# Optimization experiments

Measured on AMD Instinct MI355X. Metric: run time of the kernel, lower is better.

The kernel has to match this reference:

```python
import jax, jax.numpy as jnp
import numpy as np

N_NODES = 50000
N_EDGES = 800000
IN_FEATS = 128
OUT_CLASSES = 128


def _glorot(key, shape):
    fan_in, fan_out = shape[1], shape[0]
    limit = float(np.sqrt(6.0 / (fan_in + fan_out)))
    return jax.random.uniform(key, shape, jnp.float32, -limit, limit)


def setup_inputs() -> dict:
    key = jax.random.key(0)
    ks = jax.random.split(key, 11)
    x = jax.random.normal(ks[0], (N_NODES, IN_FEATS), jnp.float32)
    edge_index = jax.random.randint(ks[1], (2, N_EDGES), 0, N_NODES, jnp.int64)
    h = OUT_CLASSES // 2
    # PyG SAGEConv: lin_l applied to aggregated neighbors (has bias), lin_r to root (no bias)
    return {
        "x": x,
        "edge_index": edge_index,
        "W_l1": _glorot(ks[2], (OUT_CLASSES, IN_FEATS)),
        "b1": jnp.zeros((OUT_CLASSES,), jnp.float32),
        "W_r1": _glorot(ks[3], (OUT_CLASSES, IN_FEATS)),
        "W_l2": _glorot(ks[4], (h, OUT_CLASSES)),
        "b2": jnp.zeros((h,), jnp.float32),
        "W_r2": _glorot(ks[5], (h, OUT_CLASSES)),
        "W_l3": _glorot(ks[6], (OUT_CLASSES, h)),
        "b3": jnp.zeros((OUT_CLASSES,), jnp.float32),
        "W_r3": _glorot(ks[7], (OUT_CLASSES, h)),
    }


def _sage_conv(x, src, dst, W_l, b, W_r):
    # gather source-node features, mean-aggregate at destinations
    msgs = x[src]                                               # [E, d]
    agg = jax.ops.segment_sum(msgs, dst, num_segments=N_NODES)  # [N, d]
    cnt = jax.ops.segment_sum(jnp.ones((src.shape[0], 1), x.dtype), dst,
                              num_segments=N_NODES)             # [N, 1]
    mean = agg / jnp.maximum(cnt, 1.0)
    return mean @ W_l.T + b + x @ W_r.T


def reference(x, edge_index, W_l1, b1, W_r1, W_l2, b2, W_r2, W_l3, b3, W_r3):
    src, dst = edge_index[0], edge_index[1]
    h = _sage_conv(x, src, dst, W_l1, b1, W_r1)
    h = _sage_conv(h, src, dst, W_l2, b2, W_r2)
    h = _sage_conv(h, src, dst, W_l3, b3, W_r3)
    return h
```

## Files before the change

kernel.cpp:

```cpp
#include <hip/hip_runtime.h>

#define N_NODES 50000
#define N_EDGES 800000
#define BUCKETS 196
#define ECHUNK 4096
#define EBLKS 196
#define BCAP 5120

typedef __attribute__((ext_vector_type(8))) _Float16 half8;
typedef __attribute__((ext_vector_type(4))) _Float16 half4;
typedef __attribute__((ext_vector_type(4))) float f32x4;

template <int E> struct hvec;
template <> struct hvec<8> { typedef half8 t; };
template <> struct hvec<4> { typedef half4 t; };


template <int L, int E, int DEPTH>
__device__ __forceinline__ void gather_sum(const _Float16* __restrict__ feat,
                                           const unsigned short* __restrict__ csr,
                                           int start, int d, int lane,
                                           float* acc) {
  using V = typename hvec<E>::t;
  const V* ip = (const V*)feat;
  if (d <= 0) return;
  int nb = (d + DEPTH - 1) / DEPTH;
  int sc[DEPTH];
#pragma unroll
  for (int j = 0; j < DEPTH; ++j) sc[j] = csr[start + (j < d ? j : d - 1)];
  V vlast;
  for (int b = 0; b < nb; ++b) {
    V v[DEPTH];
#pragma unroll
    for (int j = 0; j < DEPTH; ++j) v[j] = ip[(size_t)sc[j] * L + lane];
    int e2 = (b + 1) * DEPTH;
    if (e2 < d) {
#pragma unroll
      for (int j = 0; j < DEPTH; ++j) {
        int idx = e2 + j;
        sc[j] = csr[start + (idx < d ? idx : d - 1)];
      }
    }
#pragma unroll
    for (int j = 0; j < DEPTH; ++j)
#pragma unroll
      for (int q = 0; q < E; ++q) acc[q] += (float)v[j][q];
    vlast = v[DEPTH - 1];
  }
  int rem = d - (nb - 1) * DEPTH;
  if (rem < DEPTH) {
    float corr = (float)(DEPTH - rem);
#pragma unroll
    for (int q = 0; q < E; ++q) acc[q] -= corr * (float)vlast[q];
  }
}


__global__ __launch_bounds__(256) void prep_k(
    const int* __restrict__ src, const int* __restrict__ dst,
    int* __restrict__ gcur, unsigned* __restrict__ binned,
    const float* __restrict__ x, _Float16* __restrict__ xh,
    const float* __restrict__ Wl1, const float* __restrict__ Wr1,
    const float* __restrict__ Wl2, const float* __restrict__ Wr2,
    const float* __restrict__ Wl3, const float* __restrict__ Wr3,
    _Float16* ph_l1, _Float16* pl_l1, _Float16* ph_r1, _Float16* pl_r1,
    _Float16* ph_c2, _Float16* pl_c2, _Float16* ph_l3, _Float16* pl_l3,
    _Float16* ph_r3, _Float16* pl_r3) {
  int blk = blockIdx.x;
  int t = threadIdx.x;
  if (blk < EBLKS) {
    __shared__ int h[BUCKETS];
    __shared__ int base[BUCKETS];
    for (int i = t; i < BUCKETS; i += 256) h[i] = 0;
    __syncthreads();
    int e0 = blk * ECHUNK;
    int eend = e0 + ECHUNK < N_EDGES ? e0 + ECHUNK : N_EDGES;
    for (int e = e0 + t; e < eend; e += 256) atomicAdd(&h[dst[e] >> 8], 1);
    __syncthreads();
    for (int i = t; i < BUCKETS; i += 256) {
      if (h[i]) base[i] = atomicAdd(&gcur[i], h[i]);
      h[i] = 0;
    }
    __syncthreads();
    for (int e = e0 + t; e < eend; e += 256) {
      int d = dst[e];
      int b = d >> 8;
      int r = atomicAdd(&h[b], 1);
      binned[(size_t)b * BCAP + base[b] + r] =
          (unsigned)src[e] | ((unsigned)(d & 255) << 16);
    }
  } else if (blk < EBLKS + 32) {
    int g = (blk - EBLKS) * 256 + t;
    const float *S0, *S1 = nullptr;
    _Float16 *ph, *pl;
    int f, K;
    if (g < 2048)      { f = g;        ph = ph_l1; pl = pl_l1; S0 = Wl1; K = 128; }
    else if (g < 4096) { f = g - 2048; ph = ph_r1; pl = pl_r1; S0 = Wr1; K = 128; }
    else if (g < 6144) { f = g - 4096; ph = ph_c2; pl = pl_c2; S0 = Wl2; S1 = Wr2; K = 128; }
    else if (g < 7168) { f = g - 6144; ph = ph_l3; pl = pl_l3; S0 = Wl3; K = 64; }
    else               { f = g - 7168; ph = ph_r3; pl = pl_r3; S0 = Wr3; K = 64; }
    int kb = f >> 9;
    int rem = f & 511;
    int n = rem >> 2;
    int lq = rem & 3;
    const float* srow =
        (S1 && n >= 64) ? (S1 + (size_t)(n - 64) * K) : (S0 + (size_t)n * K);
    int kbase = kb * 32 + lq * 8;
#pragma unroll
    for (int j = 0; j < 8; ++j) {
      float v = srow[kbase + j];
      _Float16 hi = (_Float16)v;
      ph[f * 8 + j] = hi;
      pl[f * 8 + j] = (_Float16)(v - (float)hi);
    }
  } else {
    int i = (blk - EBLKS - 32) * 256 + t;
    if (i >= N_NODES * 16) return;
    const float4* xp = (const float4*)x;
    float4 a = xp[2 * i];
    float4 b = xp[2 * i + 1];
    half8 hh;
    hh[0] = (_Float16)a.x; hh[1] = (_Float16)a.y; hh[2] = (_Float16)a.z; hh[3] = (_Float16)a.w;
    hh[4] = (_Float16)b.x; hh[5] = (_Float16)b.y; hh[6] = (_Float16)b.z; hh[7] = (_Float16)b.w;
    int node = i >> 4;
    int part = i & 15;
    ((half8*)xh)[(size_t)(part >> 2) * (N_NODES * 4) + (size_t)node * 4 + (part & 3)] = hh;
  }
}

__global__ __launch_bounds__(256) void bucket_fill_k(const unsigned* __restrict__ binned,
                                                     const int* __restrict__ gcnt,
                                                     int* __restrict__ offs,
                                                     int* __restrict__ deg,
                                                     unsigned short* __restrict__ csr) {
  __shared__ int cnt[256];
  __shared__ int loc[256];
  __shared__ int cur[256];
  int b = blockIdx.x;
  int t = threadIdx.x;
  int base = b * BCAP;
  int end = base + gcnt[b];
  cnt[t] = 0;
  __syncthreads();
  for (int e = base + t; e < end; e += 256) atomicAdd(&cnt[(binned[e] >> 16) & 255], 1);
  __syncthreads();
  loc[t] = cnt[t];
  __syncthreads();
  for (int o = 1; o < 256; o <<= 1) {
    int v = (t >= o) ? loc[t - o] : 0;
    __syncthreads();
    loc[t] += v;
    __syncthreads();
  }
  int excl = loc[t] - cnt[t];
  int node = b * 256 + t;
  if (node < N_NODES) {
    offs[node] = base + excl;
    deg[node] = cnt[t];
  }
  cur[t] = excl;
  __syncthreads();
  for (int e = base + t; e < end; e += 256) {
    unsigned r = binned[e];
    int dl = (r >> 16) & 255;
    int p = atomicAdd(&cur[dl], 1);
    csr[base + p] = (unsigned short)(r & 0xFFFF);
  }
}


template <int NSL, bool FUSE, bool OUTSL>
__global__ __launch_bounds__(256, 4) void agg_sliced_k(
    const _Float16* __restrict__ in_sl, _Float16* __restrict__ out,
    const int* __restrict__ offs, const int* __restrict__ deg,
    const unsigned short* __restrict__ csr, const float* __restrict__ bias,
    const _Float16* __restrict__ addend) {
  constexpr int COPIES = 8 / NSL;
  constexpr int F = NSL * 32;
  int g = blockIdx.x & 7;
  int s = g % NSL;
  int chunk = (blockIdx.x >> 3) * COPIES + g / NSL;
  int t = threadIdx.x;
  int node = chunk * 32 + (t >> 3);
  int lane = t & 7;
  if (node >= N_NODES) return;
  const _Float16* base = in_sl + (size_t)s * (N_NODES * 32);
  float acc[4] = {0.f, 0.f, 0.f, 0.f};
  int start = offs[node];
  int d = deg[node];
  gather_sum<8, 4, 16>(base, csr, start, d, lane, acc);
  float inv = d > 0 ? 1.0f / (float)d : 0.0f;
  int feat = s * 32 + lane * 4;
  half4 o;
  if constexpr (FUSE) {
    half4 av = *(const half4*)(addend + (size_t)node * F + feat);
#pragma unroll
    for (int q = 0; q < 4; ++q)
      o[q] = (_Float16)(acc[q] * inv + bias[feat + q] + (float)av[q]);
  } else {
#pragma unroll
    for (int q = 0; q < 4; ++q) o[q] = (_Float16)(acc[q] * inv);
  }
  _Float16* op = OUTSL ? out + (size_t)s * (N_NODES * 32) + (size_t)node * 32 + lane * 4
                       : out + (size_t)node * F + feat;
  *(half4*)op = o;
}


__global__ __launch_bounds__(256, 4) void megagemm_k(
    const _Float16* __restrict__ mh1, const _Float16* __restrict__ xsl,
    const _Float16* __restrict__ Wl1h, const _Float16* __restrict__ Wl1l,
    const _Float16* __restrict__ Wr1h, const _Float16* __restrict__ Wr1l,
    const float* __restrict__ b1,
    const _Float16* __restrict__ Wc2h, const _Float16* __restrict__ Wc2l,
    _Float16* __restrict__ Psl, _Float16* __restrict__ Rh) {
  constexpr int STR = 136;
  __shared__ _Float16 Hsm[16 * STR];
  int t = threadIdx.x;
  int wave = t >> 6;
  int lane = t & 63;
  int l15 = lane & 15;
  int lq = lane >> 4;
  int row0 = blockIdx.x * 16;
  const int woff = (l15 * 4 + lq) * 8;
  int colbase = wave * 32;
  f32x4 acc[2];
  acc[0] = (f32x4){0.f, 0.f, 0.f, 0.f};
  acc[1] = (f32x4){0.f, 0.f, 0.f, 0.f};
  {
    const _Float16* ab = mh1 + (size_t)(row0 + l15) * 128 + lq * 8;
    half8 af[4];
#pragma unroll
    for (int kb = 0; kb < 4; ++kb) af[kb] = *(const half8*)(ab + kb * 32);
#pragma unroll
    for (int kb = 0; kb < 4; ++kb)
#pragma unroll
      for (int ct = 0; ct < 2; ++ct) {
        size_t bi = (size_t)(kb * 128 + colbase + ct * 16) * 32 + woff;
        half8 bh = *(const half8*)(Wl1h + bi);
        half8 bl = *(const half8*)(Wl1l + bi);
        acc[ct] = __builtin_amdgcn_mfma_f32_16x16x32_f16(af[kb], bh, acc[ct], 0, 0, 0);
        acc[ct] = __builtin_amdgcn_mfma_f32_16x16x32_f16(af[kb], bl, acc[ct], 0, 0, 0);
      }
  }
  {
    half8 af[4];
#pragma unroll
    for (int kb = 0; kb < 4; ++kb)
      af[kb] = *(const half8*)(xsl + (size_t)kb * (N_NODES * 32) +
                               (size_t)(row0 + l15) * 32 + lq * 8);
#pragma unroll
    for (int kb = 0; kb < 4; ++kb)
#pragma unroll
      for (int ct = 0; ct < 2; ++ct) {
        size_t bi = (size_t)(kb * 128 + colbase + ct * 16) * 32 + woff;
        half8 bh = *(const half8*)(Wr1h + bi);
        half8 bl = *(const half8*)(Wr1l + bi);
        acc[ct] = __builtin_amdgcn_mfma_f32_16x16x32_f16(af[kb], bh, acc[ct], 0, 0, 0);
        acc[ct] = __builtin_amdgcn_mfma_f32_16x16x32_f16(af[kb], bl, acc[ct], 0, 0, 0);
      }
  }
#pragma unroll
  for (int r = 0; r < 4; ++r) {
    int rl = lq * 4 + r;
#pragma unroll
    for (int ct = 0; ct < 2; ++ct) {
      int col = colbase + ct * 16 + l15;
      Hsm[rl * STR + col] = (_Float16)(acc[ct][r] + b1[col]);
    }
  }
  __syncthreads();
  f32x4 a2[2];
  a2[0] = (f32x4){0.f, 0.f, 0.f, 0.f};
  a2[1] = (f32x4){0.f, 0.f, 0.f, 0.f};
  half8 af[4];
#pragma unroll
  for (int kb = 0; kb < 4; ++kb)
    af[kb] = *(const half8*)&Hsm[l15 * STR + kb * 32 + lq * 8];
#pragma unroll
  for (int kb = 0; kb < 4; ++kb)
#pragma unroll
    for (int ct = 0; ct < 2; ++ct) {
      size_t bi = (size_t)(kb * 128 + colbase + ct * 16) * 32 + woff;
      half8 bh = *(const half8*)(Wc2h + bi);
      half8 bl = *(const half8*)(Wc2l + bi);
      a2[ct] = __builtin_amdgcn_mfma_f32_16x16x32_f16(af[kb], bh, a2[ct], 0, 0, 0);
      a2[ct] = __builtin_amdgcn_mfma_f32_16x16x32_f16(af[kb], bl, a2[ct], 0, 0, 0);
    }
#pragma unroll
  for (int r = 0; r < 4; ++r) {
    int row = row0 + lq * 4 + r;
#pragma unroll
    for (int ct = 0; ct < 2; ++ct) {
      int col = colbase + ct * 16 + l15;
      float v = a2[ct][r];
      if (col < 64)
        Psl[(size_t)(col >> 5) * (N_NODES * 32) + (size_t)row * 32 + (col & 31)] =
            (_Float16)v;
      else
        Rh[(size_t)row * 64 + (col - 64)] = (_Float16)v;
    }
  }
}


__global__ __launch_bounds__(256, 2) void gemm3_k(
    const _Float16* __restrict__ mh3, const _Float16* __restrict__ h2sl,
    const _Float16* __restrict__ Wlh, const _Float16* __restrict__ Wll,
    const _Float16* __restrict__ Wrh, const _Float16* __restrict__ Wrl,
    const float* __restrict__ b3, float* __restrict__ out) {
  int wave = threadIdx.x >> 6;
  int lane = threadIdx.x & 63;
  int l15 = lane & 15;
  int lq = lane >> 4;
  int rowblk = blockIdx.x >> 1;
  int colg = blockIdx.x & 1;
  int rg = rowblk * 4 + wave;
  if (rg >= N_NODES / 16) return;
  int row0 = rg << 4;
  const int woff = (l15 * 4 + lq) * 8;
  f32x4 acc[4];
#pragma unroll
  for (int c = 0; c < 4; ++c) acc[c] = (f32x4){0.f, 0.f, 0.f, 0.f};
  {
    const _Float16* ab = mh3 + (size_t)(row0 + l15) * 64 + lq * 8;
    half8 af[2];
#pragma unroll
    for (int kb = 0; kb < 2; ++kb) af[kb] = *(const half8*)(ab + kb * 32);
#pragma unroll
    for (int kb = 0; kb < 2; ++kb)
#pragma unroll
      for (int ct = 0; ct < 4; ++ct) {
        size_t bi = (size_t)(kb * 128 + colg * 64 + ct * 16) * 32 + woff;
        half8 bh = *(const half8*)(Wlh + bi);
        half8 bl = *(const half8*)(Wll + bi);
        acc[ct] = __builtin_amdgcn_mfma_f32_16x16x32_f16(af[kb], bh, acc[ct], 0, 0, 0);
        acc[ct] = __builtin_amdgcn_mfma_f32_16x16x32_f16(af[kb], bl, acc[ct], 0, 0, 0);
      }
  }
  {
    half8 af[2];
#pragma unroll
    for (int kb = 0; kb < 2; ++kb)
      af[kb] = *(const half8*)(h2sl + (size_t)kb * (N_NODES * 32) +
                               (size_t)(row0 + l15) * 32 + lq * 8);
#pragma unroll
    for (int kb = 0; kb < 2; ++kb)
#pragma unroll
      for (int ct = 0; ct < 4; ++ct) {
        size_t bi = (size_t)(kb * 128 + colg * 64 + ct * 16) * 32 + woff;
        half8 bh = *(const half8*)(Wrh + bi);
        half8 bl = *(const half8*)(Wrl + bi);
        acc[ct] = __builtin_amdgcn_mfma_f32_16x16x32_f16(af[kb], bh, acc[ct], 0, 0, 0);
        acc[ct] = __builtin_amdgcn_mfma_f32_16x16x32_f16(af[kb], bl, acc[ct], 0, 0, 0);
      }
  }
#pragma unroll
  for (int r = 0; r < 4; ++r) {
    int row = row0 + lq * 4 + r;
#pragma unroll
    for (int ct = 0; ct < 4; ++ct) {
      int col = colg * 64 + ct * 16 + l15;
      out[(size_t)row * 128 + col] = acc[ct][r] + b3[col];
    }
  }
}

extern "C" void kernel_launch(void* const* d_in, const int* in_sizes, int n_in,
                              void* d_out, int out_size, void* d_ws, size_t ws_size,
                              hipStream_t stream) {
  const float* x   = (const float*)d_in[0];
  const int* ei    = (const int*)d_in[1];
  const float* Wl1 = (const float*)d_in[2];
  const float* b1  = (const float*)d_in[3];
  const float* Wr1 = (const float*)d_in[4];
  const float* Wl2 = (const float*)d_in[5];
  const float* b2  = (const float*)d_in[6];
  const float* Wr2 = (const float*)d_in[7];
  const float* Wl3 = (const float*)d_in[8];
  const float* b3  = (const float*)d_in[9];
  const float* Wr3 = (const float*)d_in[10];
  float* out = (float*)d_out;

  const int* src = ei;
  const int* dst = ei + N_EDGES;

  char* ws = (char*)d_ws;
  size_t off = 0;
  auto take = [&](size_t bytes) {
    void* p = ws + off;
    off += (bytes + 255) & ~(size_t)255;
    return p;
  };
  int* deg    = (int*)take((size_t)N_NODES * 4);
  int* offs   = (int*)take((size_t)N_NODES * 4);
  int* gcur   = (int*)take((size_t)BUCKETS * 4);
  unsigned* binned = (unsigned*)take((size_t)BUCKETS * BCAP * 4);
  unsigned short* csr = (unsigned short*)take((size_t)BUCKETS * BCAP * 2);
  _Float16* xh   = (_Float16*)take((size_t)N_NODES * 128 * 2);
  _Float16* mh1  = (_Float16*)take((size_t)N_NODES * 128 * 2);
  _Float16* Psl  = (_Float16*)take((size_t)N_NODES * 64 * 2);
  _Float16* Rh   = (_Float16*)take((size_t)N_NODES * 64 * 2);
  _Float16* h2sl = (_Float16*)take((size_t)N_NODES * 64 * 2);
  _Float16* mh3  = (_Float16*)take((size_t)N_NODES * 64 * 2);
  _Float16* ph_l1 = (_Float16*)take(16384 * 2);
  _Float16* pl_l1 = (_Float16*)take(16384 * 2);
  _Float16* ph_r1 = (_Float16*)take(16384 * 2);
  _Float16* pl_r1 = (_Float16*)take(16384 * 2);
  _Float16* ph_c2 = (_Float16*)take(16384 * 2);
  _Float16* pl_c2 = (_Float16*)take(16384 * 2);
  _Float16* ph_l3 = (_Float16*)take(8192 * 2);
  _Float16* pl_l3 = (_Float16*)take(8192 * 2);
  _Float16* ph_r3 = (_Float16*)take(8192 * 2);
  _Float16* pl_r3 = (_Float16*)take(8192 * 2);

  hipMemsetAsync(gcur, 0, (size_t)BUCKETS * 4, stream);

  prep_k<<<EBLKS + 32 + 3125, 256, 0, stream>>>(
      src, dst, gcur, binned, x, xh, Wl1, Wr1, Wl2, Wr2, Wl3, Wr3, ph_l1, pl_l1,
      ph_r1, pl_r1, ph_c2, pl_c2, ph_l3, pl_l3, ph_r3, pl_r3);
  bucket_fill_k<<<BUCKETS, 256, 0, stream>>>(binned, gcur, offs, deg, csr);

  agg_sliced_k<4, false, false><<<8 * 782, 256, 0, stream>>>(
      xh, mh1, offs, deg, csr, nullptr, nullptr);

  megagemm_k<<<3125, 256, 0, stream>>>(mh1, xh, ph_l1, pl_l1, ph_r1, pl_r1, b1,
                                       ph_c2, pl_c2, Psl, Rh);

  agg_sliced_k<2, true, true><<<8 * 391, 256, 0, stream>>>(
      Psl, h2sl, offs, deg, csr, b2, Rh);

  agg_sliced_k<2, false, false><<<8 * 391, 256, 0, stream>>>(
      h2sl, mh3, offs, deg, csr, nullptr, nullptr);

  gemm3_k<<<1564, 256, 0, stream>>>(mh3, h2sl, ph_l3, pl_l3, ph_r3, pl_r3, b3, out);
}
```

Measured before the change: 262.5 us.

## Split fused layer-1/layer-2 GEMM into two kernels via global h1 buffer

Replaces the fused megagemm kernel, which kept the layer-1 output tile in shared memory and fed it straight into the layer-2 projection, with two separate GEMM kernels that pass h1 through a new global fp16 buffer. Each wave now owns a 16-row by 64-column tile with no block-level sync, and launch bounds change to 2 blocks. The intent is likely to drop the __syncthreads and LDS traffic and to rebalance the MFMA work per wave. The cost is an extra kernel launch and a write plus re-read of a 50000x128 fp16 intermediate.

```diff
diff --git a/kernel.cpp b/kernel.cpp
--- a/kernel.cpp
+++ b/kernel.cpp
@@ -207,26 +207,24 @@
 }
 
 
-__global__ __launch_bounds__(256, 4) void megagemm_k(
+__global__ __launch_bounds__(256, 2) void gemm1_k(
     const _Float16* __restrict__ mh1, const _Float16* __restrict__ xsl,
-    const _Float16* __restrict__ Wl1h, const _Float16* __restrict__ Wl1l,
-    const _Float16* __restrict__ Wr1h, const _Float16* __restrict__ Wr1l,
-    const float* __restrict__ b1,
-    const _Float16* __restrict__ Wc2h, const _Float16* __restrict__ Wc2l,
-    _Float16* __restrict__ Psl, _Float16* __restrict__ Rh) {
-  constexpr int STR = 136;
-  __shared__ _Float16 Hsm[16 * STR];
-  int t = threadIdx.x;
-  int wave = t >> 6;
-  int lane = t & 63;
+    const _Float16* __restrict__ Wlh, const _Float16* __restrict__ Wll,
+    const _Float16* __restrict__ Wrh, const _Float16* __restrict__ Wrl,
+    const float* __restrict__ b1, _Float16* __restrict__ h1) {
+  int wave = threadIdx.x >> 6;
+  int lane = threadIdx.x & 63;
   int l15 = lane & 15;
   int lq = lane >> 4;
-  int row0 = blockIdx.x * 16;
+  int rowblk = blockIdx.x >> 1;
+  int colg = blockIdx.x & 1;
+  int rg = rowblk * 4 + wave;
+  if (rg >= N_NODES / 16) return;
+  int row0 = rg << 4;
   const int woff = (l15 * 4 + lq) * 8;
-  int colbase = wave * 32;
-  f32x4 acc[2];
-  acc[0] = (f32x4){0.f, 0.f, 0.f, 0.f};
-  acc[1] = (f32x4){0.f, 0.f, 0.f, 0.f};
+  f32x4 acc[4];
+#pragma unroll
+  for (int c = 0; c < 4; ++c) acc[c] = (f32x4){0.f, 0.f, 0.f, 0.f};
   {
     const _Float16* ab = mh1 + (size_t)(row0 + l15) * 128 + lq * 8;
     half8 af[4];
@@ -235,10 +233,10 @@
 #pragma unroll
     for (int kb = 0; kb < 4; ++kb)
 #pragma unroll
-      for (int ct = 0; ct < 2; ++ct) {
-        size_t bi = (size_t)(kb * 128 + colbase + ct * 16) * 32 + woff;
-        half8 bh = *(const half8*)(Wl1h + bi);
-        half8 bl = *(const half8*)(Wl1l + bi);
+      for (int ct = 0; ct < 4; ++ct) {
+        size_t bi = (size_t)(kb * 128 + colg * 64 + ct * 16) * 32 + woff;
+        half8 bh = *(const half8*)(Wlh + bi);
+        half8 bl = *(const half8*)(Wll + bi);
         acc[ct] = __builtin_amdgcn_mfma_f32_16x16x32_f16(af[kb], bh, acc[ct], 0, 0, 0);
         acc[ct] = __builtin_amdgcn_mfma_f32_16x16x32_f16(af[kb], bl, acc[ct], 0, 0, 0);
       }
@@ -252,48 +250,64 @@
 #pragma unroll
     for (int kb = 0; kb < 4; ++kb)
 #pragma unroll
-      for (int ct = 0; ct < 2; ++ct) {
-        size_t bi = (size_t)(kb * 128 + colbase + ct * 16) * 32 + woff;
-        half8 bh = *(const half8*)(Wr1h + bi);
-        half8 bl = *(const half8*)(Wr1l + bi);
+      for (int ct = 0; ct < 4; ++ct) {
+        size_t bi = (size_t)(kb * 128 + colg * 64 + ct * 16) * 32 + woff;
+        half8 bh = *(const half8*)(Wrh + bi);
+        half8 bl = *(const half8*)(Wrl + bi);
         acc[ct] = __builtin_amdgcn_mfma_f32_16x16x32_f16(af[kb], bh, acc[ct], 0, 0, 0);
         acc[ct] = __builtin_amdgcn_mfma_f32_16x16x32_f16(af[kb], bl, acc[ct], 0, 0, 0);
       }
   }
 #pragma unroll
   for (int r = 0; r < 4; ++r) {
-    int rl = lq * 4 + r;
-#pragma unroll
-    for (int ct = 0; ct < 2; ++ct) {
-      int col = colbase + ct * 16 + l15;
-      Hsm[rl * STR + col] = (_Float16)(acc[ct][r] + b1[col]);
-    }
-  }
-  __syncthreads();
-  f32x4 a2[2];
-  a2[0] = (f32x4){0.f, 0.f, 0.f, 0.f};
-  a2[1] = (f32x4){0.f, 0.f, 0.f, 0.f};
+    int row = row0 + lq * 4 + r;
+#pragma unroll
+    for (int ct = 0; ct < 4; ++ct) {
+      int col = colg * 64 + ct * 16 + l15;
+      h1[(size_t)row * 128 + col] = (_Float16)(acc[ct][r] + b1[col]);
+    }
+  }
+}
+
+
+__global__ __launch_bounds__(256, 2) void gemm2_k(
+    const _Float16* __restrict__ h1, const _Float16* __restrict__ Wh,
+    const _Float16* __restrict__ Wl, _Float16* __restrict__ Psl,
+    _Float16* __restrict__ Rh) {
+  int wave = threadIdx.x >> 6;
+  int lane = threadIdx.x & 63;
+  int l15 = lane & 15;
+  int lq = lane >> 4;
+  int rowblk = blockIdx.x >> 1;
+  int colg = blockIdx.x & 1;
+  int rg = rowblk * 4 + wave;
+  if (rg >= N_NODES / 16) return;
+  int row0 = rg << 4;
+  const int woff = (l15 * 4 + lq) * 8;
+  f32x4 acc[4];
+#pragma unroll
+  for (int c = 0; c < 4; ++c) acc[c] = (f32x4){0.f, 0.f, 0.f, 0.f};
+  const _Float16* ab = h1 + (size_t)(row0 + l15) * 128 + lq * 8;
   half8 af[4];
 #pragma unroll
+  for (int kb = 0; kb < 4; ++kb) af[kb] = *(const half8*)(ab + kb * 32);
+#pragma unroll
   for (int kb = 0; kb < 4; ++kb)
-    af[kb] = *(const half8*)&Hsm[l15 * STR + kb * 32 + lq * 8];
-#pragma unroll
-  for (int kb = 0; kb < 4; ++kb)
-#pragma unroll
-    for (int ct = 0; ct < 2; ++ct) {
-      size_t bi = (size_t)(kb * 128 + colbase + ct * 16) * 32 + woff;
-      half8 bh = *(const half8*)(Wc2h + bi);
-      half8 bl = *(const half8*)(Wc2l + bi);
-      a2[ct] = __builtin_amdgcn_mfma_f32_16x16x32_f16(af[kb], bh, a2[ct], 0, 0, 0);
-      a2[ct] = __builtin_amdgcn_mfma_f32_16x16x32_f16(af[kb], bl, a2[ct], 0, 0, 0);
+#pragma unroll
+    for (int ct = 0; ct < 4; ++ct) {
+      size_t bi = (size_t)(kb * 128 + colg * 64 + ct * 16) * 32 + woff;
+      half8 bh = *(const half8*)(Wh + bi);
+      half8 bl = *(const half8*)(Wl + bi);
+      acc[ct] = __builtin_amdgcn_mfma_f32_16x16x32_f16(af[kb], bh, acc[ct], 0, 0, 0);
+      acc[ct] = __builtin_amdgcn_mfma_f32_16x16x32_f16(af[kb], bl, acc[ct], 0, 0, 0);
     }
 #pragma unroll
   for (int r = 0; r < 4; ++r) {
     int row = row0 + lq * 4 + r;
 #pragma unroll
-    for (int ct = 0; ct < 2; ++ct) {
-      int col = colbase + ct * 16 + l15;
-      float v = a2[ct][r];
+    for (int ct = 0; ct < 4; ++ct) {
+      int col = colg * 64 + ct * 16 + l15;
+      float v = acc[ct][r];
       if (col < 64)
         Psl[(size_t)(col >> 5) * (N_NODES * 32) + (size_t)row * 32 + (col & 31)] =
             (_Float16)v;
@@ -399,6 +413,7 @@
   unsigned short* csr = (unsigned short*)take((size_t)BUCKETS * BCAP * 2);
   _Float16* xh   = (_Float16*)take((size_t)N_NODES * 128 * 2);
   _Float16* mh1  = (_Float16*)take((size_t)N_NODES * 128 * 2);
+  _Float16* h1h  = (_Float16*)take((size_t)N_NODES * 128 * 2);
   _Float16* Psl  = (_Float16*)take((size_t)N_NODES * 64 * 2);
   _Float16* Rh   = (_Float16*)take((size_t)N_NODES * 64 * 2);
   _Float16* h2sl = (_Float16*)take((size_t)N_NODES * 64 * 2);
@@ -424,8 +439,9 @@
   agg_sliced_k<4, false, false><<<8 * 782, 256, 0, stream>>>(
       xh, mh1, offs, deg, csr, nullptr, nullptr);
 
-  megagemm_k<<<3125, 256, 0, stream>>>(mh1, xh, ph_l1, pl_l1, ph_r1, pl_r1, b1,
-                                       ph_c2, pl_c2, Psl, Rh);
+  gemm1_k<<<1564, 256, 0, stream>>>(mh1, xh, ph_l1, pl_l1, ph_r1, pl_r1, b1, h1h);
+
+  gemm2_k<<<1564, 256, 0, stream>>>(h1h, ph_c2, pl_c2, Psl, Rh);
 
   agg_sliced_k<2, true, true><<<8 * 391, 256, 0, stream>>>(
       Psl, h2sl, offs, deg, csr, b2, Rh);
```

Result: slower. 270.6 us (+3.1%).
